# Kernel tuning notes

Measured on AMD Instinct MI355X. Metric: run time of the kernel, lower is better.

The kernel has to match this reference:

```python
import jax, jax.numpy as jnp
import numpy as np
from itertools import permutations

NUM_LAYERS = 3
K = 5  # fixed node degree -> every Hungarian sub-problem is 5x5
# one-hot permutation tensor: P1H[p, r, c] = 1 iff permutation p assigns row r -> col c
PERMS = np.array(list(permutations(range(K))), dtype=np.int32)          # [120, K]
P1H = (PERMS[:, :, None] == np.arange(K)[None, None, :]).astype(np.float32)  # [120, K, K]


def _mlp(x, W1, b1, W2, b2):
    # 2-layer MLP with ReLU (repo's MLP(in, hid, out, 2))
    return jax.nn.relu(x @ W1 + b1) @ W2 + b2


def _sinkhorn(src, itera):
    s = jax.nn.softmax(src, axis=1)  # row-max subtraction is built in
    for i in range(itera):
        s = s / jnp.sum(s, axis=i % 2, keepdims=True)
    return jnp.nan_to_num(s)


def _masked_softmax(src):
    s1 = jnp.nan_to_num(jax.nn.softmax(src, axis=1))
    s2 = jnp.nan_to_num(jax.nn.softmax(src, axis=0))
    return (s1 + s2) * 0.5


def setup_inputs() -> dict:
    key = jax.random.key(0)
    ks = jax.random.split(key, 12)
    n1 = n2 = 1024
    hid = 64
    adj1 = jax.random.randint(ks[0], (n1, K), 0, n1)
    adj2 = jax.random.randint(ks[1], (n2, K), 0, n2)
    # adjacency matrices consistent with the neighbor lists
    G1 = jnp.zeros((n1, n1), jnp.float32).at[jnp.arange(n1)[:, None], adj1].set(1.0)
    G2 = jnp.zeros((n2, n2), jnp.float32).at[jnp.arange(n2)[:, None], adj2].set(1.0)
    s = 0.1
    return {
        'G1': G1, 'G2': G2, 'adj1': adj1, 'adj2': adj2,
        'ro_W1': jax.random.normal(ks[2], (NUM_LAYERS, 1, hid), jnp.float32) * s,
        'ro_b1': jax.random.normal(ks[3], (NUM_LAYERS, hid), jnp.float32) * s,
        'ro_W2': jax.random.normal(ks[4], (NUM_LAYERS, hid, 1), jnp.float32) * s,
        'ro_b2': jax.random.normal(ks[5], (NUM_LAYERS, 1), jnp.float32) * s,
        'fin_W1': jax.random.normal(ks[6], (1, hid), jnp.float32) * s,
        'fin_b1': jax.random.normal(ks[7], (hid,), jnp.float32) * s,
        'fin_W2': jax.random.normal(ks[8], (hid, 1), jnp.float32) * s,
        'fin_b2': jax.random.normal(ks[9], (1,), jnp.float32) * s,
    }


def reference(G1, G2, adj1, adj2, ro_W1, ro_b1, ro_W2, ro_b2, fin_W1, fin_b1, fin_W2, fin_b2):
    n1 = G1.shape[0]
    n2 = G2.shape[0]
    d1 = jnp.sum(G1, axis=1)
    d2 = jnp.sum(G2, axis=1)
    ttheta = jnp.mean(d1)
    # S[i, j, 0] = -|d1[i] - d2[j]|
    S = -jnp.abs(d1[:, None] - d2[None, :])[..., None]  # [n1, n2, 1]
    p1h = jnp.asarray(P1H)
    for li in range(NUM_LAYERS):
        Wn = _sinkhorn(_mlp(S / ttheta, ro_W1[li], ro_b1[li], ro_W2[li], ro_b2[li]).squeeze(-1), 5)
        W = jnp.log(Wn * (n1 * 1.5))
        W = jnp.where(jnp.isneginf(W), jnp.float32(-1e12), W)
        W = jnp.where(jnp.isposinf(W), jnp.float32(1e12), W)
        Wd = jax.lax.stop_gradient(W)  # matches W.detach().numpy()
        # small[a, b, r, c] = Wd[adj1[a, r], adj2[b, c]]  -> [n1, n2, K, K]
        small = jnp.transpose(Wd[adj1][:, :, adj2], (0, 2, 1, 3))
        # exact linear_sum_assignment(-small): maximize sum over the K! permutations
        scores = jnp.einsum('abrc,prc->abp', small, p1h)  # [n1, n2, 120]
        X1 = jnp.max(scores, axis=-1)                      # [n1, n2]
        S = X1[..., None]
    out = _masked_softmax(_mlp(S, fin_W1, fin_b1, fin_W2, fin_b2).squeeze(-1))
    return out
```

## Files before the change

### kernel.cpp

```cpp
#include <hip/hip_runtime.h>
#include <math.h>

#define N 1024
#define NB 256
#define KD 5
#define SL 8
#define NT 126
#define NTP 136
#define MAGIC 0x13572468
#define FSTRIDE 32
#define NGO 32
#define FREGION (NB * FSTRIDE + NGO * FSTRIDE)


__device__ __forceinline__ float load_sc(const float* p){
  return __hip_atomic_load(p, __ATOMIC_RELAXED, __HIP_MEMORY_SCOPE_AGENT);
}
__device__ __forceinline__ void store_sc(float* p, float v){
  __hip_atomic_store(p, v, __ATOMIC_RELAXED, __HIP_MEMORY_SCOPE_AGENT);
}
__device__ __forceinline__ int load_sci(const int* p){
  return __hip_atomic_load(p, __ATOMIC_RELAXED, __HIP_MEMORY_SCOPE_AGENT);
}
__device__ __forceinline__ void store_sci(int* p, int v){
  __hip_atomic_store(p, v, __ATOMIC_RELAXED, __HIP_MEMORY_SCOPE_AGENT);
}

__device__ __forceinline__ void gbar_arrive(int* flg){
  __builtin_amdgcn_s_waitcnt(0);
  __syncthreads();
  if (blockIdx.x != 0 && threadIdx.x == 0)
    store_sci(&flg[blockIdx.x * FSTRIDE], MAGIC);
}
__device__ __forceinline__ void gbar_wait(int* flg){
  const int t = threadIdx.x, B = blockIdx.x;
  int* go = flg + NB * FSTRIDE;
  if (B == 0){
    if (t > 0 && t < NB){
      while (load_sci(&flg[t * FSTRIDE]) != MAGIC) __builtin_amdgcn_s_sleep(1);
    }
    __syncthreads();
    if (t < NGO) store_sci(&go[t * FSTRIDE], MAGIC);
  } else {
    if (t == 0){
      while (load_sci(&go[(B & (NGO - 1)) * FSTRIDE]) != MAGIC) __builtin_amdgcn_s_sleep(1);
    }
    __syncthreads();
  }
}
__device__ __forceinline__ void gbarS(int* flg){ gbar_arrive(flg); gbar_wait(flg); }

__device__ __forceinline__ float wred_sum(float v){
#pragma unroll
  for (int off = 32; off > 0; off >>= 1) v += __shfl_down(v, off);
  return v;
}
__device__ __forceinline__ void bsum4(float v[4], float* s64){
  float w0 = wred_sum(v[0]), w1 = wred_sum(v[1]), w2 = wred_sum(v[2]), w3 = wred_sum(v[3]);
  __syncthreads();
  int wv = threadIdx.x >> 6;
  if ((threadIdx.x & 63) == 0){ s64[wv*4] = w0; s64[wv*4+1] = w1; s64[wv*4+2] = w2; s64[wv*4+3] = w3; }
  __syncthreads();
  float r0 = 0.f, r1 = 0.f, r2 = 0.f, r3 = 0.f;
  const float4* s4 = (const float4*)s64;
#pragma unroll
  for (int i = 0; i < 16; ++i){
    float4 vv = s4[i];
    r0 += vv.x; r1 += vv.y; r2 += vv.z; r3 += vv.w;
  }
  v[0] = r0; v[1] = r1; v[2] = r2; v[3] = r3;
}

__device__ __forceinline__ int distinct5(const int* v){
  int c = 0;
#pragma unroll
  for (int r = 0; r < KD; ++r){
    bool dup = false;
#pragma unroll
    for (int s = 0; s < r; ++s) dup = dup || (v[s] == v[r]);
    c += dup ? 0 : 1;
  }
  return c;
}
__device__ __forceinline__ void sort5(int* s){
#pragma unroll
  for (int i = 0; i < 4; ++i)
#pragma unroll
    for (int j = 0; j < 4 - i; ++j){
      int a = s[j], b = s[j+1];
      s[j] = min(a, b); s[j+1] = max(a, b);
    }
}
__device__ __forceinline__ int msrank(const int* c5){
  const int C_[6][5] = { {0,0,0,0,0},
                         {1,1,1,1,1},
                         {1,2,3,4,5},
                         {1,3,6,10,15},
                         {1,4,10,20,35},
                         {1,5,15,35,70} };
  int rank = 0, prev = 0;
#pragma unroll
  for (int i = 0; i < 5; ++i){
    for (int v = prev; v < c5[i]; ++v) rank += C_[5 - v][4 - i];
    prev = c5[i];
  }
  return rank;
}

#define DP5(ACCESS, OUT) {                                        \
  float f[32]; f[0] = 0.f;                                        \
  _Pragma("unroll")                                               \
  for (int r = 0; r < KD; ++r){                                   \
    float tr[KD];                                                 \
    _Pragma("unroll")                                             \
    for (int c = 0; c < KD; ++c) tr[c] = (ACCESS);                \
    _Pragma("unroll")                                             \
    for (int m = 1; m < 32; ++m){                                 \
      if (__popc(m) == r + 1){                                    \
        float dpb = 0.f; bool dpi = true;                         \
        _Pragma("unroll")                                         \
        for (int c = 0; c < KD; ++c)                              \
          if (m & (1 << c)){                                      \
            float dpv = f[m ^ (1 << c)] + tr[c];                  \
            dpb = dpi ? dpv : fmaxf(dpb, dpv);                    \
            dpi = false;                                          \
          }                                                       \
        f[m] = dpb;                                               \
      }                                                           \
    }                                                             \
  }                                                               \
  OUT = f[31];                                                    \
}

__device__ __forceinline__ void pwl_build(int t,
    const float* __restrict__ w1g, const float* __restrict__ b1g,
    const float* __restrict__ w2g, const float* __restrict__ b2g,
    float* ux, float* udA, float* udB,
    float* xss, float* dAs, float* dBs,
    float* Atb, float* Btb, float* sA0B0)
{
  if (t < 64){
    float w1 = w1g[t], bb = b1g[t], w2v = w2g[t];
    float xk, sdA, sdB, a0t = 0.f, b0t = 0.f;
    if (w1 != 0.f){
      xk = -bb / w1;
      float dA = w1 * w2v, dB = bb * w2v;
      if (w1 > 0.f){ sdA = dA;  sdB = dB; }
      else         { sdA = -dA; sdB = -dB; a0t = dA; b0t = dB; }
    } else {
      xk = 3.0e38f; sdA = 0.f; sdB = 0.f;
      b0t = fmaxf(bb, 0.f) * w2v;
    }
    ux[t] = xk; udA[t] = sdA; udB[t] = sdB;
    float A0 = wred_sum(a0t);
    float B0 = wred_sum(b0t);
    if (t == 0){ sA0B0[0] = A0; sA0B0[1] = B0 + b2g[0]; }
  }
  __syncthreads();
  if (t < 64){
    float xk = ux[t]; int rank = 0;
    for (int j = 0; j < 64; ++j){
      float xj = ux[j];
      rank += (xj < xk || (xj == xk && j < t)) ? 1 : 0;
    }
    xss[rank] = ux[t]; dAs[rank] = udA[t]; dBs[rank] = udB[t];
  }
  __syncthreads();
  if (t < 65){
    float sa = sA0B0[0], sb = sA0B0[1];
    for (int r = 0; r < t; ++r){ sa += dAs[r]; sb += dBs[r]; }
    Atb[t] = sa; Btb[t] = sb;
  }
  __syncthreads();
}

__global__ __launch_bounds__(1024) void
kFused(const int* __restrict__ adj1, const int* __restrict__ adj2,
       const float* __restrict__ roW1, const float* __restrict__ roB1,
       const float* __restrict__ roW2, const float* __restrict__ roB2,
       const float* __restrict__ fW1, const float* __restrict__ fB1,
       const float* __restrict__ fW2, const float* __restrict__ fB2,
       float* __restrict__ tY1g,
       float* __restrict__ C1B, float* __restrict__ C2B, float* __restrict__ C3B,
       float* __restrict__ CFB, float* __restrict__ Rg,
       float* __restrict__ outp,
       int* __restrict__ flg)
{
  __shared__ __align__(16) char uS[20 * N * 4 + N * 4];
  float* tY1 = (float*)uS;
  float (*rows20)[N] = (float (*)[N])uS;
  float* lc = (float*)(uS + 20 * N * 4);
  __shared__ unsigned char t2c[NT][5];
  __shared__ unsigned char sg1[N], sg2[N];
  __shared__ unsigned short st1[N], st2[N];
  __shared__ int h1[8], h2[8];
  __shared__ int cnt1T[NT], cnt2T[NT];
  __shared__ float A1[NT], B1[NT];
  __shared__ float sY0[25], slR0[5], slC0[5], stt2[2];
  __shared__ float slR1[NT], slC1[NT];
  __shared__ float vq[NT], vC[NT], vqi[NT], vCi[NT];
  __shared__ __align__(16) float s64[64];
  __shared__ float sAv[4];
  __shared__ float ux[64], udA[64], udB[64], xss[64], dAs[64], dBs[64];
  __shared__ float Atb[65], Btb[65], sA0B0[2];
  __shared__ float xs3[64], A3t[65], B3t[65];

  const int t = threadIdx.x, B = blockIdx.x;
  const float L1536 = logf(1536.0f);

  if (t < 8){ h1[t] = 0; h2[t] = 0; }
  if (t < NT){ cnt1T[t] = 0; cnt2T[t] = 0; }
#pragma unroll 1
  for (int key = t; key < 3125; key += 1024){
    int d[5]; int k2 = key;
#pragma unroll
    for (int i = 0; i < 5; ++i){ d[i] = k2 % 5; k2 /= 5; }
    if (d[0] <= d[1] && d[1] <= d[2] && d[2] <= d[3] && d[3] <= d[4]){
      int r = msrank(d);
#pragma unroll
      for (int i = 0; i < 5; ++i) t2c[r][i] = (unsigned char)d[i];
    }
  }
  int a2[KD], a1v[KD];
#pragma unroll
  for (int c = 0; c < KD; ++c) a2[c] = adj2[t * KD + c];
#pragma unroll
  for (int r = 0; r < KD; ++r) a1v[r] = adj1[t * KD + r];
  {
    int c2 = distinct5(a2) - 1, c1 = distinct5(a1v) - 1;
    sg2[t] = (unsigned char)c2; sg1[t] = (unsigned char)c1;
#pragma unroll
    for (int k = 0; k < 5; ++k){
      unsigned long long m1 = __ballot(c1 == k);
      unsigned long long m2 = __ballot(c2 == k);
      if ((t & 63) == 0){
        if (m1) atomicAdd(&h1[k], (int)__popcll(m1));
        if (m2) atomicAdd(&h2[k], (int)__popcll(m2));
      }
    }
  }
  __syncthreads();

  {
    int c5[KD];
#pragma unroll
    for (int r = 0; r < KD; ++r) c5[r] = sg1[a1v[r]];
    sort5(c5);
    int ty = msrank(c5);
    st1[t] = (unsigned short)ty; atomicAdd(&cnt1T[ty], 1);
  }
  {
    int c5[KD];
#pragma unroll
    for (int c = 0; c < KD; ++c) c5[c] = sg2[a2[c]];
    sort5(c5);
// ... 79 lines not shown
      stt2[0] = tt;
    }
  } else if (t < 128){
    int l = t - 64;
    const float* w1g = roW1 + 64;
    const float* b1g = roB1 + 64;
    const float* w2g = roW2 + 64;
    const float* b2g = roB2 + 1;
    float w1 = w1g[l], bb = b1g[l], w2v = w2g[l];
    float xk, sdA, sdB, a0t = 0.f, b0t = 0.f;
    if (w1 != 0.f){
      xk = -bb / w1;
      float dA = w1 * w2v, dB = bb * w2v;
      if (w1 > 0.f){ sdA = dA;  sdB = dB; }
      else         { sdA = -dA; sdB = -dB; a0t = dA; b0t = dB; }
    } else {
      xk = 3.0e38f; sdA = 0.f; sdB = 0.f;
      b0t = fmaxf(bb, 0.f) * w2v;
    }
    ux[l] = xk; udA[l] = sdA; udB[l] = sdB;
    float A0 = wred_sum(a0t);
    float B0 = wred_sum(b0t);
    if (l == 0){ sA0B0[0] = A0; sA0B0[1] = B0 + b2g[0]; }
  }
  __syncthreads();

  if (t < 64){
    float xk = ux[t]; int rank = 0;
    for (int j = 0; j < 64; ++j){
      float xj = ux[j];
      rank += (xj < xk || (xj == xk && j < t)) ? 1 : 0;
    }
    xss[rank] = ux[t]; dAs[rank] = udA[t]; dBs[rank] = udB[t];
  } else if (t >= 256 && t < 256 + NT){
    int ty = t - 256;
    float sa = 5.0f * L1536, sb = 0.f;
#pragma unroll
    for (int i = 0; i < KD; ++i){
      int cl = t2c[ty][i];
      sa += slR0[cl];
      sb -= slC0[cl];
    }
    A1[ty] = sa; B1[ty] = sb;
  }
  __syncthreads();
  if (t < 65){
    float sa = sA0B0[0], sb = sA0B0[1];
    for (int r = 0; r < t; ++r){ sa += dAs[r]; sb += dBs[r]; }
    Atb[t] = sa; Btb[t] = sb;
  }
  __syncthreads();

  const float tt = stt2[0];
  if (t < 63){
    int e = B + 256 * t;
    if (e < NT * NT){
      int tau = e / NT, ups = e - tau * NT;
      const unsigned char* G = t2c[tau];
      const unsigned char* H = t2c[ups];
      float D;
      DP5(sY0[(int)G[r] * 5 + (int)H[c]], D);
      float x = (A1[tau] + B1[ups] + D) / tt;
      int seg = 0;
#pragma unroll
      for (int s = 64; s; s >>= 1)
        if (seg + s <= 64 && xss[seg + s - 1] <= x) seg += s;
      store_sc(&tY1g[e], fmaf(Atb[seg], x, Btb[seg]));
    }
  }

  gbar_arrive(flg + 0 * FREGION);
  pwl_build(t, fW1, fB1, fW2, fB2,
            ux, udA, udB, xs3, dAs, dBs, A3t, B3t, sA0B0);
  pwl_build(t, roW1 + 128, roB1 + 128, roW2 + 128, roB2 + 2,
            ux, udA, udB, xss, dAs, dBs, Atb, Btb, sA0B0);
  gbar_wait(flg + 0 * FREGION);

  float rv[16];
  int lidx[16];
#pragma unroll
  for (int i = 0; i < 16; ++i){
    int e = t + 1024 * i;
    if (e < NT * NT){
      rv[i] = load_sc(&tY1g[e]);
      lidx[i] = e + (NTP - NT) * (e / NT);
    }
  }
#pragma unroll
  for (int i = 0; i < 16; ++i){
    int e = t + 1024 * i;
    if (e < NT * NT) tY1[lidx[i]] = rv[i];
  }
  __syncthreads();

  int stc[KD];
#pragma unroll
  for (int c = 0; c < KD; ++c) stc[c] = st2[a2[c]];
  float D2[4];
#pragma unroll 1
  for (int rr = 0; rr < 4; ++rr){
    int str_[KD];
#pragma unroll
    for (int r = 0; r < KD; ++r) str_[r] = st1[adj1[(4 * B + rr) * KD + r]];
    float D;
    DP5(tY1[str_[r] * NTP + stc[c]], D);
    D2[rr] = D;
  }
  __syncthreads();
#pragma unroll
  for (int i = 0; i < 16; ++i){
    int e = t + 1024 * i;
    if (e < NT * NT) tY1[lidx[i]] = expf(rv[i]);
  }
  __syncthreads();

  {
    int g = t >> 3, j = t & 7;
    float Er[16], Ec[16];
    if (g < NT){
#pragma unroll
      for (int i = 0; i < 16; ++i){
        int u = j + 8 * i;
        if (u < NT){
          Er[i] = (float)cnt2T[u] * tY1[g * NTP + u];
          Ec[i] = (float)cnt1T[u] * tY1[u * NTP + g];
        } else { Er[i] = 0.f; Ec[i] = 0.f; }
      }
    }
    if (g < NT){
      float acc = 0.f;
#pragma unroll
      for (int i = 0; i < 16; ++i){ int u = j + 8 * i; if (u < NT) acc += Er[i]; }
      acc += __shfl_down(acc, 4, 8); acc += __shfl_down(acc, 2, 8); acc += __shfl_down(acc, 1, 8);
      if (j == 0){ vq[g] = acc; vqi[g] = 1.0f / acc; }
    }
    __syncthreads();
    if (g < NT){
      float acc = 0.f;
#pragma unroll
      for (int i = 0; i < 16; ++i){ int u = j + 8 * i; if (u < NT) acc += Ec[i] * vqi[u]; }
      acc += __shfl_down(acc, 4, 8); acc += __shfl_down(acc, 2, 8); acc += __shfl_down(acc, 1, 8);
      if (j == 0){ vC[g] = acc; vCi[g] = 1.0f / acc; }
    }
    __syncthreads();
    if (g < NT){
      float acc = 0.f;
#pragma unroll
      for (int i = 0; i < 16; ++i){ int u = j + 8 * i; if (u < NT) acc += Er[i] * vCi[u]; }
      acc += __shfl_down(acc, 4, 8); acc += __shfl_down(acc, 2, 8); acc += __shfl_down(acc, 1, 8);
      if (j == 0){ vq[g] = acc; vqi[g] = 1.0f / acc; }
    }
    __syncthreads();
    if (g < NT){
      float acc = 0.f;
#pragma unroll
      for (int i = 0; i < 16; ++i){ int u = j + 8 * i; if (u < NT) acc += Ec[i] * vqi[u]; }
      acc += __shfl_down(acc, 4, 8); acc += __shfl_down(acc, 2, 8); acc += __shfl_down(acc, 1, 8);
      if (j == 0){ vC[g] = acc; vCi[g] = 1.0f / acc; }
    }
    __syncthreads();
    if (g < NT){
      float acc = 0.f;
#pragma unroll
      for (int i = 0; i < 16; ++i){ int u = j + 8 * i; if (u < NT) acc += Er[i] * vCi[u]; }
      acc += __shfl_down(acc, 4, 8); acc += __shfl_down(acc, 2, 8); acc += __shfl_down(acc, 1, 8);
      if (j == 0){ vq[g] = acc; vqi[g] = 1.0f / acc; }
    }
    __syncthreads();
    if (g < NT){
      float acc = 0.f;
#pragma unroll
      for (int i = 0; i < 16; ++i){ int u = j + 8 * i; if (u < NT) acc += Ec[i] * vqi[u]; }
      acc += __shfl_down(acc, 4, 8); acc += __shfl_down(acc, 2, 8); acc += __shfl_down(acc, 1, 8);
      if (j == 0) vC[g] = acc;
    }
    __syncthreads();
  }
  if (t < NT){ slR1[t] = -logf(vq[t]); slC1[t] = logf(vC[t]); }
  __syncthreads();

  if (t < 4){
    int a = 4 * B + t;
    float s = 5.0f * L1536;
#pragma unroll
    for (int r = 0; r < KD; ++r) s += slR1[st1[adj1[a * KD + r]]];
    sAv[t] = s;
  }
  float Bv2 = 0.f;
#pragma unroll
  for (int c = 0; c < KD; ++c) Bv2 -= slC1[stc[c]];
  __syncthreads();

  float y2[4];
#pragma unroll
  for (int rr = 0; rr < 4; ++rr){
    float x = (sAv[rr] + Bv2 + D2[rr]) / tt;
    int seg = 0;
#pragma unroll
    for (int s = 64; s; s >>= 1)
      if (seg + s <= 64 && xss[seg + s - 1] <= x) seg += s;
    y2[rr] = fmaf(Atb[seg], x, Btb[seg]);
  }
  float E[4], q4[4];
#pragma unroll
  for (int r = 0; r < 4; ++r){ E[r] = expf(y2[r]); q4[r] = E[r]; }
  bsum4(q4, s64);
  {
    float cp = 0.f;
#pragma unroll
    for (int r = 0; r < 4; ++r){
      store_sc(&outp[(size_t)(4 * B + r) * N + t], y2[r]);
      cp += E[r] / q4[r];
    }
    atomicAdd(&C1B[(size_t)(B & (SL - 1)) * N + t], cp);
  }

  gbarS(flg + 1 * FREGION);

  float rv20[20];
#pragma unroll
  for (int k = 0; k < 20; ++k){
    int src = adj1[(4 * B + (k / 5)) * KD + (k % 5)];
    rv20[k] = load_sc(&outp[(size_t)src * N + t]);
  }

  {
    float C = 0.f;
#pragma unroll
    for (int k = 0; k < SL; ++k) C += load_sc(&C1B[(size_t)k * N + t]);
    float iC = 1.0f / C;
#pragma unroll
    for (int r = 0; r < 4; ++r) q4[r] = E[r] * iC;
    bsum4(q4, s64);
    float cp = 0.f;
#pragma unroll
    for (int r = 0; r < 4; ++r) cp += E[r] / q4[r];
    atomicAdd(&C2B[(size_t)(B & (SL - 1)) * N + t], cp);
  }

  gbar_arrive(flg + 2 * FREGION);
#pragma unroll
  for (int k = 0; k < 20; ++k) rows20[k][t] = rv20[k];
  __syncthreads();
  float D3[4];
#pragma unroll 1
  for (int rr = 0; rr < 4; ++rr){
    float D;
    DP5(rows20[rr * 5 + r][a2[c]], D);
    D3[rr] = D;
  }
  gbar_wait(flg + 2 * FREGION);

  {
    float C = 0.f;
#pragma unroll
    for (int k = 0; k < SL; ++k) C += load_sc(&C2B[(size_t)k * N + t]);
    float iC = 1.0f / C;
#pragma unroll
    for (int r = 0; r < 4; ++r) q4[r] = E[r] * iC;
    bsum4(q4, s64);
    float cp = 0.f;
#pragma unroll
    for (int r = 0; r < 4; ++r) cp += E[r] / q4[r];
    if (t < 4) store_sc(&Rg[4 * B + t], 1.0f / q4[t]);
    atomicAdd(&C3B[(size_t)(B & (SL - 1)) * N + t], cp);
  }

  gbarS(flg + 3 * FREGION);
  {
    float C = 0.f;
#pragma unroll
    for (int k = 0; k < SL; ++k) C += load_sc(&C3B[(size_t)k * N + t]);
    lc[t] = logf(C);
  }
  if (t >= 64 && t < 68){
    int a = 4 * B + (t - 64);
    float s = 5.0f * logf(1536.0f);
#pragma unroll
    for (int r = 0; r < KD; ++r) s += logf(load_sc(&Rg[adj1[a * KD + r]]));
    sAv[t - 64] = s;
  }
  __syncthreads();

  float Bvl = 0.f;
#pragma unroll
  for (int c = 0; c < KD; ++c) Bvl -= lc[a2[c]];

  float y[4];
#pragma unroll
  for (int rr = 0; rr < 4; ++rr){
    float x = sAv[rr] + Bvl + D3[rr];
    int seg = 0;
#pragma unroll
    for (int s = 64; s; s >>= 1)
      if (seg + s <= 64 && xs3[seg + s - 1] <= x) seg += s;
    y[rr] = fmaf(A3t[seg], x, B3t[seg]);
  }

  float e4[4];
#pragma unroll
  for (int r = 0; r < 4; ++r){ e4[r] = expf(y[r]); q4[r] = e4[r]; }
  bsum4(q4, s64);

  {
    float cp = 0.f;
#pragma unroll
    for (int r = 0; r < 4; ++r) cp += e4[r];
    atomicAdd(&CFB[(size_t)(B & (SL - 1)) * N + t], cp);
  }

  gbar_arrive(flg + 4 * FREGION);
  float iq[4];
#pragma unroll
  for (int r = 0; r < 4; ++r) iq[r] = 1.0f / q4[r];
  gbar_wait(flg + 4 * FREGION);

  float CF = 0.f;
#pragma unroll
  for (int k = 0; k < SL; ++k) CF += load_sc(&CFB[(size_t)k * N + t]);
  float iCF = 1.0f / CF;
#pragma unroll
  for (int r = 0; r < 4; ++r){
    float v = 0.5f * e4[r] * (iq[r] + iCF);
    outp[(size_t)(4 * B + r) * N + t] = v;
  }
}

extern "C" void kernel_launch(void* const* d_in, const int* in_sizes, int n_in,
                              void* d_out, int out_size, void* d_ws, size_t ws_size,
                              hipStream_t stream){
  (void)in_sizes; (void)n_in; (void)out_size; (void)ws_size;
  const int*   adj1 = (const int*)d_in[2];
  const int*   adj2 = (const int*)d_in[3];
  const float* roW1 = (const float*)d_in[4];
  const float* roB1 = (const float*)d_in[5];
  const float* roW2 = (const float*)d_in[6];
  const float* roB2 = (const float*)d_in[7];
  const float* fW1  = (const float*)d_in[8];
  const float* fB1  = (const float*)d_in[9];
  const float* fW2  = (const float*)d_in[10];
  const float* fB2  = (const float*)d_in[11];
  float* out = (float*)d_out;

  float* Pp   = (float*)d_ws;
  float* Rg   = Pp + (size_t)4 * SL * N;
  float* tY1g = Rg + N;
  int*   flg  = (int*)(tY1g + NT * NT);

  kFused<<<NB, 1024, 0, stream>>>(adj1, adj2, roW1, roB1, roW2, roB2,
                                  fW1, fB1, fW2, fB2,
                                  tY1g,
                                  Pp + (size_t)0 * SL * N, Pp + (size_t)1 * SL * N,
                                  Pp + (size_t)2 * SL * N, Pp + (size_t)3 * SL * N,
                                  Rg, out, flg);
}
```

Before: 146.9 us.

## Double grid to 512 blocks with two rows each and shrink shared memory

Raises the persistent grid from 256 to 512 blocks, so each block now handles two output rows instead of four. Shared memory is cut by dropping the padded tY1 layout, shrinking the row buffer and aliasing several small arrays, so two 1024-thread blocks can fit per CU. The intent is more parallelism and less serial per-block work on a 256-CU GPU. In exchange, the global barriers must wait on twice as many blocks, there are more atomic adds, and removing the padding may bring back LDS bank conflicts.

```diff
diff --git a/kernel.cpp b/kernel.cpp
--- a/kernel.cpp
+++ b/kernel.cpp
@@ -2,11 +2,10 @@
 #include <math.h>
 
 #define N 1024
-#define NB 256
+#define NB 512
 #define KD 5
 #define SL 8
 #define NT 126
-#define NTP 136
 #define MAGIC 0x13572468
 #define FSTRIDE 32
 #define NGO 32
@@ -55,20 +54,17 @@
   for (int off = 32; off > 0; off >>= 1) v += __shfl_down(v, off);
   return v;
 }
-__device__ __forceinline__ void bsum4(float v[4], float* s64){
-  float w0 = wred_sum(v[0]), w1 = wred_sum(v[1]), w2 = wred_sum(v[2]), w3 = wred_sum(v[3]);
+__device__ __forceinline__ void bsum2(float v[2], float* s64){
+  float w0 = wred_sum(v[0]), w1 = wred_sum(v[1]);
   __syncthreads();
   int wv = threadIdx.x >> 6;
-  if ((threadIdx.x & 63) == 0){ s64[wv*4] = w0; s64[wv*4+1] = w1; s64[wv*4+2] = w2; s64[wv*4+3] = w3; }
-  __syncthreads();
-  float r0 = 0.f, r1 = 0.f, r2 = 0.f, r3 = 0.f;
-  const float4* s4 = (const float4*)s64;
-#pragma unroll
-  for (int i = 0; i < 16; ++i){
-    float4 vv = s4[i];
-    r0 += vv.x; r1 += vv.y; r2 += vv.z; r3 += vv.w;
-  }
-  v[0] = r0; v[1] = r1; v[2] = r2; v[3] = r3;
+  if ((threadIdx.x & 63) == 0){ s64[wv*2] = w0; s64[wv*2+1] = w1; }
+  __syncthreads();
+  float r0 = 0.f, r1 = 0.f;
+  const float2* s2 = (const float2*)s64;
+#pragma unroll
+  for (int i = 0; i < 16; ++i){ float2 vv = s2[i]; r0 += vv.x; r1 += vv.y; }
+  v[0] = r0; v[1] = r1;
 }
 
 __device__ __forceinline__ int distinct5(const int* v){
@@ -174,7 +170,7 @@
   __syncthreads();
 }
 
-__global__ __launch_bounds__(1024) void
+__global__ __launch_bounds__(1024, 8) void
 kFused(const int* __restrict__ adj1, const int* __restrict__ adj2,
        const float* __restrict__ roW1, const float* __restrict__ roB1,
        const float* __restrict__ roW2, const float* __restrict__ roB2,
@@ -186,21 +182,27 @@
        float* __restrict__ outp,
        int* __restrict__ flg)
 {
-  __shared__ __align__(16) char uS[20 * N * 4 + N * 4];
+  __shared__ __align__(16) char uS[NT * NT * 4];
   float* tY1 = (float*)uS;
-  float (*rows20)[N] = (float (*)[N])uS;
-  float* lc = (float*)(uS + 20 * N * 4);
+  float (*rows10)[N] = (float (*)[N])uS;
+  float* lc = (float*)(uS + 10 * N * 4);
+  __shared__ __align__(16) unsigned char sgU[2048];
+  unsigned char* sg1 = sgU;
+  unsigned char* sg2 = sgU + 1024;
+  float* vq  = (float*)sgU;
+  float* vC  = vq + NT;
+  float* vqi = vC + NT;
+  float* vCi = vqi + NT;
+  __shared__ float AB1U[2 * NT];
+  float* A1 = AB1U;         float* B1 = AB1U + NT;
+  float* slR1 = AB1U;       float* slC1 = AB1U + NT;
   __shared__ unsigned char t2c[NT][5];
-  __shared__ unsigned char sg1[N], sg2[N];
   __shared__ unsigned short st1[N], st2[N];
   __shared__ int h1[8], h2[8];
   __shared__ int cnt1T[NT], cnt2T[NT];
-  __shared__ float A1[NT], B1[NT];
   __shared__ float sY0[25], slR0[5], slC0[5], stt2[2];
-  __shared__ float slR1[NT], slC1[NT];
-  __shared__ float vq[NT], vC[NT], vqi[NT], vCi[NT];
   __shared__ __align__(16) float s64[64];
-  __shared__ float sAv[4];
+  __shared__ float sAv[2];
   __shared__ float ux[64], udA[64], udB[64], xss[64], dAs[64], dBs[64];
   __shared__ float Atb[65], Btb[65], sA0B0[2];
   __shared__ float xs3[64], A3t[65], B3t[65];
@@ -386,8 +388,8 @@
   __syncthreads();
 
   const float tt = stt2[0];
-  if (t < 63){
-    int e = B + 256 * t;
+  if (t < 32){
+    int e = B + 512 * t;
     if (e < NT * NT){
       int tau = e / NT, ups = e - tau * NT;
       const unsigned char* G = t2c[tau];
@@ -411,40 +413,36 @@
   gbar_wait(flg + 0 * FREGION);
 
   float rv[16];
-  int lidx[16];
 #pragma unroll
   for (int i = 0; i < 16; ++i){
     int e = t + 1024 * i;
-    if (e < NT * NT){
-      rv[i] = load_sc(&tY1g[e]);
-      lidx[i] = e + (NTP - NT) * (e / NT);
-    }
+    if (e < NT * NT) rv[i] = load_sc(&tY1g[e]);
   }
 #pragma unroll
   for (int i = 0; i < 16; ++i){
     int e = t + 1024 * i;
-    if (e < NT * NT) tY1[lidx[i]] = rv[i];
+    if (e < NT * NT) tY1[e] = rv[i];
   }
   __syncthreads();
 
   int stc[KD];
 #pragma unroll
   for (int c = 0; c < KD; ++c) stc[c] = st2[a2[c]];
-  float D2[4];
+  float D2[2];
 #pragma unroll 1
-  for (int rr = 0; rr < 4; ++rr){
+  for (int rr = 0; rr < 2; ++rr){
     int str_[KD];
 #pragma unroll
-    for (int r = 0; r < KD; ++r) str_[r] = st1[adj1[(4 * B + rr) * KD + r]];
+    for (int r = 0; r < KD; ++r) str_[r] = st1[adj1[(2 * B + rr) * KD + r]];
     float D;
-    DP5(tY1[str_[r] * NTP + stc[c]], D);
+    DP5(tY1[str_[r] * NT + stc[c]], D);
     D2[rr] = D;
   }
   __syncthreads();
 #pragma unroll
   for (int i = 0; i < 16; ++i){
     int e = t + 1024 * i;
-    if (e < NT * NT) tY1[lidx[i]] = expf(rv[i]);
+    if (e < NT * NT) tY1[e] = expf(rv[i]);
   }
   __syncthreads();
 
@@ -456,8 +454,8 @@
       for (int i = 0; i < 16; ++i){
         int u = j + 8 * i;
         if (u < NT){
-          Er[i] = (float)cnt2T[u] * tY1[g * NTP + u];
-          Ec[i] = (float)cnt1T[u] * tY1[u * NTP + g];
+          Er[i] = (float)cnt2T[u] * tY1[g * NT + u];
+          Ec[i] = (float)cnt1T[u] * tY1[u * NT + g];
         } else { Er[i] = 0.f; Ec[i] = 0.f; }
       }
     }
@@ -513,8 +511,8 @@
   if (t < NT){ slR1[t] = -logf(vq[t]); slC1[t] = logf(vC[t]); }
   __syncthreads();
 
-  if (t < 4){
-    int a = 4 * B + t;
+  if (t < 2){
+    int a = 2 * B + t;
     float s = 5.0f * L1536;
 #pragma unroll
     for (int r = 0; r < KD; ++r) s += slR1[st1[adj1[a * KD + r]]];
@@ -525,9 +523,9 @@
   for (int c = 0; c < KD; ++c) Bv2 -= slC1[stc[c]];
   __syncthreads();
 
-  float y2[4];
-#pragma unroll
-  for (int rr = 0; rr < 4; ++rr){
+  float y2[2];
+#pragma unroll
+  for (int rr = 0; rr < 2; ++rr){
     float x = (sAv[rr] + Bv2 + D2[rr]) / tt;
     int seg = 0;
 #pragma unroll
@@ -535,15 +533,15 @@
       if (seg + s <= 64 && xss[seg + s - 1] <= x) seg += s;
     y2[rr] = fmaf(Atb[seg], x, Btb[seg]);
   }
-  float E[4], q4[4];
-#pragma unroll
-  for (int r = 0; r < 4; ++r){ E[r] = expf(y2[r]); q4[r] = E[r]; }
-  bsum4(q4, s64);
+  float E[2], q4[2];
+#pragma unroll
+  for (int r = 0; r < 2; ++r){ E[r] = expf(y2[r]); q4[r] = E[r]; }
+  bsum2(q4, s64);
   {
     float cp = 0.f;
 #pragma unroll
-    for (int r = 0; r < 4; ++r){
-      store_sc(&outp[(size_t)(4 * B + r) * N + t], y2[r]);
+    for (int r = 0; r < 2; ++r){
+      store_sc(&outp[(size_t)(2 * B + r) * N + t], y2[r]);
       cp += E[r] / q4[r];
     }
     atomicAdd(&C1B[(size_t)(B & (SL - 1)) * N + t], cp);
@@ -551,11 +549,11 @@
 
   gbarS(flg + 1 * FREGION);
 
-  float rv20[20];
-#pragma unroll
-  for (int k = 0; k < 20; ++k){
-    int src = adj1[(4 * B + (k / 5)) * KD + (k % 5)];
-    rv20[k] = load_sc(&outp[(size_t)src * N + t]);
+  float rv10[10];
+#pragma unroll
+  for (int k = 0; k < 10; ++k){
+    int src = adj1[(2 * B + (k / 5)) * KD + (k % 5)];
+    rv10[k] = load_sc(&outp[(size_t)src * N + t]);
   }
 
   {
@@ -564,23 +562,23 @@
     for (int k = 0; k < SL; ++k) C += load_sc(&C1B[(size_t)k * N + t]);
     float iC = 1.0f / C;
 #pragma unroll
-    for (int r = 0; r < 4; ++r) q4[r] = E[r] * iC;
-    bsum4(q4, s64);
+    for (int r = 0; r < 2; ++r) q4[r] = E[r] * iC;
+    bsum2(q4, s64);
     float cp = 0.f;
 #pragma unroll
-    for (int r = 0; r < 4; ++r) cp += E[r] / q4[r];
+    for (int r = 0; r < 2; ++r) cp += E[r] / q4[r];
     atomicAdd(&C2B[(size_t)(B & (SL - 1)) * N + t], cp);
   }
 
   gbar_arrive(flg + 2 * FREGION);
 #pragma unroll
-  for (int k = 0; k < 20; ++k) rows20[k][t] = rv20[k];
-  __syncthreads();
-  float D3[4];
+  for (int k = 0; k < 10; ++k) rows10[k][t] = rv10[k];
+  __syncthreads();
+  float D3[2];
 #pragma unroll 1
-  for (int rr = 0; rr < 4; ++rr){
+  for (int rr = 0; rr < 2; ++rr){
     float D;
-    DP5(rows20[rr * 5 + r][a2[c]], D);
+    DP5(rows10[rr * 5 + r][a2[c]], D);
     D3[rr] = D;
   }
   gbar_wait(flg + 2 * FREGION);
@@ -591,12 +589,12 @@
     for (int k = 0; k < SL; ++k) C += load_sc(&C2B[(size_t)k * N + t]);
     float iC = 1.0f / C;
 #pragma unroll
-    for (int r = 0; r < 4; ++r) q4[r] = E[r] * iC;
-    bsum4(q4, s64);
+    for (int r = 0; r < 2; ++r) q4[r] = E[r] * iC;
+    bsum2(q4, s64);
     float cp = 0.f;
 #pragma unroll
-    for (int r = 0; r < 4; ++r) cp += E[r] / q4[r];
-    if (t < 4) store_sc(&Rg[4 * B + t], 1.0f / q4[t]);
+    for (int r = 0; r < 2; ++r) cp += E[r] / q4[r];
+    if (t < 2) store_sc(&Rg[2 * B + t], 1.0f / q4[t]);
     atomicAdd(&C3B[(size_t)(B & (SL - 1)) * N + t], cp);
   }
 
@@ -607,8 +605,8 @@
     for (int k = 0; k < SL; ++k) C += load_sc(&C3B[(size_t)k * N + t]);
     lc[t] = logf(C);
   }
-  if (t >= 64 && t < 68){
-    int a = 4 * B + (t - 64);
+  if (t >= 64 && t < 66){
+    int a = 2 * B + (t - 64);
     float s = 5.0f * logf(1536.0f);
 #pragma unroll
     for (int r = 0; r < KD; ++r) s += logf(load_sc(&Rg[adj1[a * KD + r]]));
@@ -620,9 +618,9 @@
 #pragma unroll
   for (int c = 0; c < KD; ++c) Bvl -= lc[a2[c]];
 
-  float y[4];
-#pragma unroll
-  for (int rr = 0; rr < 4; ++rr){
+  float y[2];
+#pragma unroll
+  for (int rr = 0; rr < 2; ++rr){
     float x = sAv[rr] + Bvl + D3[rr];
     int seg = 0;
 #pragma unroll
@@ -631,22 +629,22 @@
     y[rr] = fmaf(A3t[seg], x, B3t[seg]);
   }
 
-  float e4[4];
-#pragma unroll
-  for (int r = 0; r < 4; ++r){ e4[r] = expf(y[r]); q4[r] = e4[r]; }
-  bsum4(q4, s64);
+  float e4[2];
+#pragma unroll
+  for (int r = 0; r < 2; ++r){ e4[r] = expf(y[r]); q4[r] = e4[r]; }
+  bsum2(q4, s64);
 
   {
     float cp = 0.f;
 #pragma unroll
-    for (int r = 0; r < 4; ++r) cp += e4[r];
+    for (int r = 0; r < 2; ++r) cp += e4[r];
     atomicAdd(&CFB[(size_t)(B & (SL - 1)) * N + t], cp);
   }
 
   gbar_arrive(flg + 4 * FREGION);
-  float iq[4];
-#pragma unroll
-  for (int r = 0; r < 4; ++r) iq[r] = 1.0f / q4[r];
+  float iq[2];
+#pragma unroll
+  for (int r = 0; r < 2; ++r) iq[r] = 1.0f / q4[r];
   gbar_wait(flg + 4 * FREGION);
 
   float CF = 0.f;
@@ -654,9 +652,9 @@
   for (int k = 0; k < SL; ++k) CF += load_sc(&CFB[(size_t)k * N + t]);
   float iCF = 1.0f / CF;
 #pragma unroll
-  for (int r = 0; r < 4; ++r){
+  for (int r = 0; r < 2; ++r){
     float v = 0.5f * e4[r] * (iq[r] + iCF);
-    outp[(size_t)(4 * B + r) * N + t] = v;
+    outp[(size_t)(2 * B + r) * N + t] = v;
   }
 }
 
```

After: 169.6 us. 1.15x slower.

## Add 512-block persistent kernel variant with two rows per block

Applied to the files above, without the earlier changes.

Adds a second fused kernel that launches 512 blocks of 1024 threads. Each block handles two rows instead of four, register use is capped at 64 VGPRs, and shared memory is cut so two blocks can fit per CU. The host queries occupancy and picks this variant when two blocks can be resident, otherwise it falls back to the original 256-block kernel. The aim is to double resident waves and halve per-block serial work. The cost is a larger grid barrier (512 flags polled by block 0), plus risk of register spills or a deadlock if the occupancy query overstates residency.

```diff
diff --git a/kernel.cpp b/kernel.cpp
--- a/kernel.cpp
+++ b/kernel.cpp
@@ -2,7 +2,6 @@
 #include <math.h>
 
 #define N 1024
-#define NB 256
 #define KD 5
 #define SL 8
 #define NT 126
@@ -10,7 +9,8 @@
 #define MAGIC 0x13572468
 #define FSTRIDE 32
 #define NGO 32
-#define FREGION (NB * FSTRIDE + NGO * FSTRIDE)
+#define FREG512 (512 * FSTRIDE + NGO * FSTRIDE)
+#define FREG256 (256 * FSTRIDE + NGO * FSTRIDE)
 
 
 __device__ __forceinline__ float load_sc(const float* p){
@@ -32,11 +32,11 @@
   if (blockIdx.x != 0 && threadIdx.x == 0)
     store_sci(&flg[blockIdx.x * FSTRIDE], MAGIC);
 }
-__device__ __forceinline__ void gbar_wait(int* flg){
+__device__ __forceinline__ void gbar_wait(int* flg, int nb){
   const int t = threadIdx.x, B = blockIdx.x;
-  int* go = flg + NB * FSTRIDE;
+  int* go = flg + nb * FSTRIDE;
   if (B == 0){
-    if (t > 0 && t < NB){
+    if (t > 0 && t < nb){
       while (load_sci(&flg[t * FSTRIDE]) != MAGIC) __builtin_amdgcn_s_sleep(1);
     }
     __syncthreads();
@@ -48,12 +48,23 @@
     __syncthreads();
   }
 }
-__device__ __forceinline__ void gbarS(int* flg){ gbar_arrive(flg); gbar_wait(flg); }
 
 __device__ __forceinline__ float wred_sum(float v){
 #pragma unroll
   for (int off = 32; off > 0; off >>= 1) v += __shfl_down(v, off);
   return v;
+}
+__device__ __forceinline__ void bsum2(float v[2], float* s64){
+  float w0 = wred_sum(v[0]), w1 = wred_sum(v[1]);
+  __syncthreads();
+  int wv = threadIdx.x >> 6;
+  if ((threadIdx.x & 63) == 0){ s64[wv*2] = w0; s64[wv*2+1] = w1; }
+  __syncthreads();
+  float r0 = 0.f, r1 = 0.f;
+  const float2* s2 = (const float2*)s64;
+#pragma unroll
+  for (int i = 0; i < 16; ++i){ float2 vv = s2[i]; r0 += vv.x; r1 += vv.y; }
+  v[0] = r0; v[1] = r1;
 }
 __device__ __forceinline__ void bsum4(float v[4], float* s64){
   float w0 = wred_sum(v[0]), w1 = wred_sum(v[1]), w2 = wred_sum(v[2]), w3 = wred_sum(v[3]);
@@ -174,17 +185,510 @@
   __syncthreads();
 }
 
+
+__global__ __launch_bounds__(1024) __attribute__((amdgpu_num_vgpr(64))) void
+kF512(const int* __restrict__ adj1, const int* __restrict__ adj2,
+      const float* __restrict__ roW1, const float* __restrict__ roB1,
+      const float* __restrict__ roW2, const float* __restrict__ roB2,
+      const float* __restrict__ fW1, const float* __restrict__ fB1,
+      const float* __restrict__ fW2, const float* __restrict__ fB2,
+      float* __restrict__ tY1g,
+      float* __restrict__ C1B, float* __restrict__ C2B, float* __restrict__ C3B,
+      float* __restrict__ CFB, float* __restrict__ Rg,
+      float* __restrict__ outp,
+      int* __restrict__ flg)
+{
+  __shared__ __align__(16) char uS[NT * NT * 4];
+  float* tY1 = (float*)uS;
+  float (*rows10)[N] = (float (*)[N])uS;
+  float* lc = (float*)(uS + 10 * N * 4);
+  __shared__ __align__(16) unsigned char sgU[2048];
+  unsigned char* sg1 = sgU;
+  unsigned char* sg2 = sgU + 1024;
+  float* vq  = (float*)sgU;
+  float* vC  = vq + NT;
+  float* vqi = vC + NT;
+  float* vCi = vqi + NT;
+  __shared__ float AB1U[2 * NT];
+  float* A1 = AB1U;         float* B1 = AB1U + NT;
+  float* slR1 = AB1U;       float* slC1 = AB1U + NT;
+  __shared__ unsigned char t2c[NT][5];
+  __shared__ unsigned short st1[N], st2[N];
+  __shared__ int h1[8], h2[8];
+  __shared__ int cnt1T[NT], cnt2T[NT];
+  __shared__ float sY0[25], slR0[5], slC0[5], stt2[2];
+  __shared__ __align__(16) float s64[64];
+  __shared__ float sAv[2];
+  __shared__ float ux[64], udA[64], udB[64], xss[64], dAs[64], dBs[64];
+  __shared__ float Atb[65], Btb[65], sA0B0[2];
+  __shared__ float xs3[64], A3t[65], B3t[65];
+
+  const int t = threadIdx.x, B = blockIdx.x;
+  const float L1536 = logf(1536.0f);
+
+  if (t < 8){ h1[t] = 0; h2[t] = 0; }
+  if (t < NT){ cnt1T[t] = 0; cnt2T[t] = 0; }
+#pragma unroll 1
+  for (int key = t; key < 3125; key += 1024){
+    int d[5]; int k2 = key;
+#pragma unroll
+    for (int i = 0; i < 5; ++i){ d[i] = k2 % 5; k2 /= 5; }
+    if (d[0] <= d[1] && d[1] <= d[2] && d[2] <= d[3] && d[3] <= d[4]){
+      int r = msrank(d);
+#pragma unroll
+      for (int i = 0; i < 5; ++i) t2c[r][i] = (unsigned char)d[i];
+    }
+  }
+  int a2[KD], a1v[KD];
+#pragma unroll
+  for (int c = 0; c < KD; ++c) a2[c] = adj2[t * KD + c];
+#pragma unroll
+  for (int r = 0; r < KD; ++r) a1v[r] = adj1[t * KD + r];
+  {
+    int c2 = distinct5(a2) - 1, c1 = distinct5(a1v) - 1;
+    sg2[t] = (unsigned char)c2; sg1[t] = (unsigned char)c1;
+#pragma unroll
+    for (int k = 0; k < 5; ++k){
+      unsigned long long m1 = __ballot(c1 == k);
+      unsigned long long m2 = __ballot(c2 == k);
+      if ((t & 63) == 0){
+        if (m1) atomicAdd(&h1[k], (int)__popcll(m1));
+        if (m2) atomicAdd(&h2[k], (int)__popcll(m2));
+      }
+    }
+  }
+  __syncthreads();
+
+  {
+    int c5[KD];
+#pragma unroll
+    for (int r = 0; r < KD; ++r) c5[r] = sg1[a1v[r]];
+    sort5(c5);
+    int ty = msrank(c5);
+    st1[t] = (unsigned short)ty; atomicAdd(&cnt1T[ty], 1);
+  }
+  {
+    int c5[KD];
+#pragma unroll
+    for (int c = 0; c < KD; ++c) c5[c] = sg2[a2[c]];
+    sort5(c5);
+    int ty = msrank(c5);
+    st2[t] = (unsigned short)ty; atomicAdd(&cnt2T[ty], 1);
+  }
+
+  if (t < 64){
+    float cnt1[5], cnt2[5];
+#pragma unroll
+    for (int g = 0; g < 5; ++g){ cnt1[g] = (float)h1[g]; cnt2[g] = (float)h2[g]; }
+    float tt = 0.f;
+#pragma unroll
+    for (int g = 0; g < 5; ++g) tt += (float)(g + 1) * cnt1[g];
+    tt *= (1.0f / 1024.0f);
+    float tab[5];
+#pragma unroll 1
+    for (int i = 0; i < 5; ++i){
+      float x = -(float)i / tt;
+      float acc = roB2[0];
+      for (int k = 0; k < 64; ++k){
+        float hh = fmaxf(fmaf(x, roW1[k], roB1[k]), 0.f);
+        acc = fmaf(hh, roW2[k], acc);
+      }
+      tab[i] = acc;
+    }
+    float Ee[5][5];
+#pragma unroll
+    for (int g = 0; g < 5; ++g)
+#pragma unroll
+      for (int h = 0; h < 5; ++h) Ee[g][h] = expf(tab[abs(g - h)]);
+    float q0[5], C1c[5], q1[5], C2c[5], q2[5], C3c[5];
+#pragma unroll
+    for (int g = 0; g < 5; ++g){
+      float s = 0.f;
+#pragma unroll
+      for (int h = 0; h < 5; ++h) s += cnt2[h] * Ee[g][h];
+      q0[g] = s;
+    }
+#pragma unroll
+    for (int h = 0; h < 5; ++h){
+      float s = 0.f;
+#pragma unroll
+      for (int g = 0; g < 5; ++g) s += cnt1[g] * Ee[g][h] / q0[g];
+      C1c[h] = s;
+    }
+#pragma unroll
+    for (int g = 0; g < 5; ++g){
+      float s = 0.f;
+#pragma unroll
+      for (int h = 0; h < 5; ++h) s += cnt2[h] * Ee[g][h] / C1c[h];
+      q1[g] = s;
+    }
+#pragma unroll
+    for (int h = 0; h < 5; ++h){
+      float s = 0.f;
+#pragma unroll
+      for (int g = 0; g < 5; ++g) s += cnt1[g] * Ee[g][h] / q1[g];
+      C2c[h] = s;
+    }
+#pragma unroll
+    for (int g = 0; g < 5; ++g){
+      float s = 0.f;
+#pragma unroll
+      for (int h = 0; h < 5; ++h) s += cnt2[h] * Ee[g][h] / C2c[h];
+      q2[g] = s;
+    }
+#pragma unroll
+    for (int h = 0; h < 5; ++h){
+      float s = 0.f;
+#pragma unroll
+      for (int g = 0; g < 5; ++g) s += cnt1[g] * Ee[g][h] / q2[g];
+      C3c[h] = s;
+    }
+    if (t == 0){
+#pragma unroll
+      for (int g = 0; g < 5; ++g){
+#pragma unroll
+        for (int h = 0; h < 5; ++h) sY0[g * 5 + h] = tab[abs(g - h)];
+        slR0[g] = -logf(q2[g]);
+        slC0[g] = logf(C3c[g]);
+      }
+      stt2[0] = tt;
+    }
+  } else if (t < 128){
+    int l = t - 64;
+    const float* w1g = roW1 + 64;
+    const float* b1g = roB1 + 64;
+    const float* w2g = roW2 + 64;
+    const float* b2g = roB2 + 1;
+    float w1 = w1g[l], bb = b1g[l], w2v = w2g[l];
+    float xk, sdA, sdB, a0t = 0.f, b0t = 0.f;
+    if (w1 != 0.f){
+      xk = -bb / w1;
+      float dA = w1 * w2v, dB = bb * w2v;
+      if (w1 > 0.f){ sdA = dA;  sdB = dB; }
+      else         { sdA = -dA; sdB = -dB; a0t = dA; b0t = dB; }
+    } else {
+      xk = 3.0e38f; sdA = 0.f; sdB = 0.f;
+      b0t = fmaxf(bb, 0.f) * w2v;
+    }
+    ux[l] = xk; udA[l] = sdA; udB[l] = sdB;
+    float A0 = wred_sum(a0t);
+    float B0 = wred_sum(b0t);
+    if (l == 0){ sA0B0[0] = A0; sA0B0[1] = B0 + b2g[0]; }
+  }
+  __syncthreads();
+
+  if (t < 64){
+    float xk = ux[t]; int rank = 0;
+    for (int j = 0; j < 64; ++j){
+      float xj = ux[j];
+      rank += (xj < xk || (xj == xk && j < t)) ? 1 : 0;
+    }
+    xss[rank] = ux[t]; dAs[rank] = udA[t]; dBs[rank] = udB[t];
+  } else if (t >= 256 && t < 256 + NT){
+    int ty = t - 256;
+    float sa = 5.0f * L1536, sb = 0.f;
+#pragma unroll
+    for (int i = 0; i < KD; ++i){
+      int cl = t2c[ty][i];
+      sa += slR0[cl];
+      sb -= slC0[cl];
+    }
+    A1[ty] = sa; B1[ty] = sb;
+  }
+  __syncthreads();
+  if (t < 65){
+    float sa = sA0B0[0], sb = sA0B0[1];
+    for (int r = 0; r < t; ++r){ sa += dAs[r]; sb += dBs[r]; }
+    Atb[t] = sa; Btb[t] = sb;
+  }
+  __syncthreads();
+
+  const float tt = stt2[0];
+  if (t < 32){
+    int e = B + 512 * t;
+    if (e < NT * NT){
+      int tau = e / NT, ups = e - tau * NT;
+      const unsigned char* G = t2c[tau];
+      const unsigned char* H = t2c[ups];
+      float D;
+      DP5(sY0[(int)G[r] * 5 + (int)H[c]], D);
+      float x = (A1[tau] + B1[ups] + D) / tt;
+      int seg = 0;
+#pragma unroll
+      for (int s = 64; s; s >>= 1)
+        if (seg + s <= 64 && xss[seg + s - 1] <= x) seg += s;
+      store_sc(&tY1g[e], fmaf(Atb[seg], x, Btb[seg]));
+    }
+  }
+
+  gbar_arrive(flg + 0 * FREG512);
+  pwl_build(t, fW1, fB1, fW2, fB2,
+            ux, udA, udB, xs3, dAs, dBs, A3t, B3t, sA0B0);
+  pwl_build(t, roW1 + 128, roB1 + 128, roW2 + 128, roB2 + 2,
+            ux, udA, udB, xss, dAs, dBs, Atb, Btb, sA0B0);
+  gbar_wait(flg + 0 * FREG512, 512);
+
+  {
+    float rv[16];
+#pragma unroll
+    for (int i = 0; i < 16; ++i){
+      int e = t + 1024 * i;
+      if (e < NT * NT) rv[i] = load_sc(&tY1g[e]);
+    }
+#pragma unroll
+    for (int i = 0; i < 16; ++i){
+      int e = t + 1024 * i;
+      if (e < NT * NT) tY1[e] = rv[i];
+    }
+  }
+  __syncthreads();
+
+  int stc[KD];
+#pragma unroll
+  for (int c = 0; c < KD; ++c) stc[c] = st2[a2[c]];
+  float D2[2];
+#pragma unroll 1
+  for (int rr = 0; rr < 2; ++rr){
+    int str_[KD];
+#pragma unroll
+    for (int r = 0; r < KD; ++r) str_[r] = st1[adj1[(2 * B + rr) * KD + r]];
+    float D;
+    DP5(tY1[str_[r] * NT + stc[c]], D);
+    D2[rr] = D;
+  }
+  __syncthreads();
+#pragma unroll
+  for (int i = 0; i < 16; ++i){
+    int e = t + 1024 * i;
+    if (e < NT * NT){ float lv = tY1[e]; tY1[e] = expf(lv); }
+  }
+  __syncthreads();
+
+  {
+    int g = t >> 3, j = t & 7;
+    float Er[16], Ec[16];
+    if (g < NT){
+#pragma unroll
+      for (int i = 0; i < 16; ++i){
+        int u = j + 8 * i;
+        if (u < NT){
+          Er[i] = (float)cnt2T[u] * tY1[g * NT + u];
+          Ec[i] = (float)cnt1T[u] * tY1[u * NT + g];
+        } else { Er[i] = 0.f; Ec[i] = 0.f; }
+      }
+    }
+    if (g < NT){
+      float acc = 0.f;
+#pragma unroll
+      for (int i = 0; i < 16; ++i){ int u = j + 8 * i; if (u < NT) acc += Er[i]; }
+      acc += __shfl_down(acc, 4, 8); acc += __shfl_down(acc, 2, 8); acc += __shfl_down(acc, 1, 8);
+      if (j == 0){ vq[g] = acc; vqi[g] = 1.0f / acc; }
+    }
+    __syncthreads();
+    if (g < NT){
+      float acc = 0.f;
+#pragma unroll
+      for (int i = 0; i < 16; ++i){ int u = j + 8 * i; if (u < NT) acc += Ec[i] * vqi[u]; }
+      acc += __shfl_down(acc, 4, 8); acc += __shfl_down(acc, 2, 8); acc += __shfl_down(acc, 1, 8);
+      if (j == 0){ vC[g] = acc; vCi[g] = 1.0f / acc; }
+    }
+    __syncthreads();
+    if (g < NT){
+      float acc = 0.f;
+#pragma unroll
+      for (int i = 0; i < 16; ++i){ int u = j + 8 * i; if (u < NT) acc += Er[i] * vCi[u]; }
+      acc += __shfl_down(acc, 4, 8); acc += __shfl_down(acc, 2, 8); acc += __shfl_down(acc, 1, 8);
+      if (j == 0){ vq[g] = acc; vqi[g] = 1.0f / acc; }
+    }
+    __syncthreads();
+    if (g < NT){
+      float acc = 0.f;
+#pragma unroll
+      for (int i = 0; i < 16; ++i){ int u = j + 8 * i; if (u < NT) acc += Ec[i] * vqi[u]; }
+      acc += __shfl_down(acc, 4, 8); acc += __shfl_down(acc, 2, 8); acc += __shfl_down(acc, 1, 8);
+      if (j == 0){ vC[g] = acc; vCi[g] = 1.0f / acc; }
+    }
+    __syncthreads();
+    if (g < NT){
+      float acc = 0.f;
+#pragma unroll
+      for (int i = 0; i < 16; ++i){ int u = j + 8 * i; if (u < NT) acc += Er[i] * vCi[u]; }
+      acc += __shfl_down(acc, 4, 8); acc += __shfl_down(acc, 2, 8); acc += __shfl_down(acc, 1, 8);
+      if (j == 0){ vq[g] = acc; vqi[g] = 1.0f / acc; }
+    }
+    __syncthreads();
+    if (g < NT){
+      float acc = 0.f;
+#pragma unroll
+      for (int i = 0; i < 16; ++i){ int u = j + 8 * i; if (u < NT) acc += Ec[i] * vqi[u]; }
+      acc += __shfl_down(acc, 4, 8); acc += __shfl_down(acc, 2, 8); acc += __shfl_down(acc, 1, 8);
+      if (j == 0) vC[g] = acc;
+    }
+    __syncthreads();
+  }
+  if (t < NT){ slR1[t] = -logf(vq[t]); slC1[t] = logf(vC[t]); }
+  __syncthreads();
+
+  if (t < 2){
+    int a = 2 * B + t;
+    float s = 5.0f * L1536;
+#pragma unroll
+    for (int r = 0; r < KD; ++r) s += slR1[st1[adj1[a * KD + r]]];
+    sAv[t] = s;
+  }
+  float Bv2 = 0.f;
+#pragma unroll
+  for (int c = 0; c < KD; ++c) Bv2 -= slC1[stc[c]];
+  __syncthreads();
+
+  float y2[2];
+#pragma unroll
+  for (int rr = 0; rr < 2; ++rr){
+    float x = (sAv[rr] + Bv2 + D2[rr]) / tt;
+    int seg = 0;
+#pragma unroll
+    for (int s = 64; s; s >>= 1)
+      if (seg + s <= 64 && xss[seg + s - 1] <= x) seg += s;
+    y2[rr] = fmaf(Atb[seg], x, Btb[seg]);
+  }
+  float E[2], q4[2];
+#pragma unroll
+  for (int r = 0; r < 2; ++r){ E[r] = expf(y2[r]); q4[r] = E[r]; }
+  bsum2(q4, s64);
+  {
+    float cp = 0.f;
+#pragma unroll
+    for (int r = 0; r < 2; ++r){
+      store_sc(&outp[(size_t)(2 * B + r) * N + t], y2[r]);
+      cp += E[r] / q4[r];
+    }
+    atomicAdd(&C1B[(size_t)(B & (SL - 1)) * N + t], cp);
+  }
+
+  gbar_arrive(flg + 1 * FREG512);
+  gbar_wait(flg + 1 * FREG512, 512);
+
+  float rv10[10];
+#pragma unroll
+  for (int k = 0; k < 10; ++k){
+    int src = adj1[(2 * B + (k / 5)) * KD + (k % 5)];
+    rv10[k] = load_sc(&outp[(size_t)src * N + t]);
+  }
+
+  {
+    float C = 0.f;
+#pragma unroll
+    for (int k = 0; k < SL; ++k) C += load_sc(&C1B[(size_t)k * N + t]);
+    float iC = 1.0f / C;
+#pragma unroll
+    for (int r = 0; r < 2; ++r) q4[r] = E[r] * iC;
+    bsum2(q4, s64);
+    float cp = 0.f;
+#pragma unroll
+    for (int r = 0; r < 2; ++r) cp += E[r] / q4[r];
+    atomicAdd(&C2B[(size_t)(B & (SL - 1)) * N + t], cp);
+  }
+
+  gbar_arrive(flg + 2 * FREG512);
+#pragma unroll
+  for (int k = 0; k < 10; ++k) rows10[k][t] = rv10[k];
+  __syncthreads();
+  float D3[2];
+#pragma unroll 1
+  for (int rr = 0; rr < 2; ++rr){
+    float D;
+    DP5(rows10[rr * 5 + r][a2[c]], D);
+    D3[rr] = D;
+  }
+  gbar_wait(flg + 2 * FREG512, 512);
+
+  {
+    float C = 0.f;
+#pragma unroll
+    for (int k = 0; k < SL; ++k) C += load_sc(&C2B[(size_t)k * N + t]);
+    float iC = 1.0f / C;
+#pragma unroll
+    for (int r = 0; r < 2; ++r) q4[r] = E[r] * iC;
+    bsum2(q4, s64);
+    float cp = 0.f;
+#pragma unroll
+    for (int r = 0; r < 2; ++r) cp += E[r] / q4[r];
+    if (t < 2) store_sc(&Rg[2 * B + t], 1.0f / q4[t]);
+    atomicAdd(&C3B[(size_t)(B & (SL - 1)) * N + t], cp);
+  }
+
+  gbar_arrive(flg + 3 * FREG512);
+  gbar_wait(flg + 3 * FREG512, 512);
+  {
+    float C = 0.f;
+#pragma unroll
+    for (int k = 0; k < SL; ++k) C += load_sc(&C3B[(size_t)k * N + t]);
+    lc[t] = logf(C);
+  }
+  if (t >= 64 && t < 66){
+    int a = 2 * B + (t - 64);
+    float s = 5.0f * logf(1536.0f);
+#pragma unroll
+    for (int r = 0; r < KD; ++r) s += logf(load_sc(&Rg[adj1[a * KD + r]]));
+    sAv[t - 64] = s;
+  }
+  __syncthreads();
+
+  float Bvl = 0.f;
+#pragma unroll
+  for (int c = 0; c < KD; ++c) Bvl -= lc[a2[c]];
+
+  float y[2];
+#pragma unroll
+  for (int rr = 0; rr < 2; ++rr){
+    float x = sAv[rr] + Bvl + D3[rr];
+    int seg = 0;
+#pragma unroll
+    for (int s = 64; s; s >>= 1)
+      if (seg + s <= 64 && xs3[seg + s - 1] <= x) seg += s;
+    y[rr] = fmaf(A3t[seg], x, B3t[seg]);
+  }
+
+  float e4[2];
+#pragma unroll
+  for (int r = 0; r < 2; ++r){ e4[r] = expf(y[r]); q4[r] = e4[r]; }
+  bsum2(q4, s64);
+
+  {
+    float cp = 0.f;
+#pragma unroll
+    for (int r = 0; r < 2; ++r) cp += e4[r];
+    atomicAdd(&CFB[(size_t)(B & (SL - 1)) * N + t], cp);
+  }
+
+  gbar_arrive(flg + 4 * FREG512);
+  float iq[2];
+#pragma unroll
+  for (int r = 0; r < 2; ++r) iq[r] = 1.0f / q4[r];
+  gbar_wait(flg + 4 * FREG512, 512);
+
+  float CF = 0.f;
+#pragma unroll
+  for (int k = 0; k < SL; ++k) CF += load_sc(&CFB[(size_t)k * N + t]);
+  float iCF = 1.0f / CF;
+#pragma unroll
+  for (int r = 0; r < 2; ++r){
+    float v = 0.5f * e4[r] * (iq[r] + iCF);
+    outp[(size_t)(2 * B + r) * N + t] = v;
+  }
+}
+
 __global__ __launch_bounds__(1024) void
-kFused(const int* __restrict__ adj1, const int* __restrict__ adj2,
-       const float* __restrict__ roW1, const float* __restrict__ roB1,
-       const float* __restrict__ roW2, const float* __restrict__ roB2,
-       const float* __restrict__ fW1, const float* __restrict__ fB1,
-       const float* __restrict__ fW2, const float* __restrict__ fB2,
-       float* __restrict__ tY1g,
-       float* __restrict__ C1B, float* __restrict__ C2B, float* __restrict__ C3B,
-       float* __restrict__ CFB, float* __restrict__ Rg,
-       float* __restrict__ outp,
-       int* __restrict__ flg)
+kF256(const int* __restrict__ adj1, const int* __restrict__ adj2,
+      const float* __restrict__ roW1, const float* __restrict__ roB1,
+      const float* __restrict__ roW2, const float* __restrict__ roB2,
+      const float* __restrict__ fW1, const float* __restrict__ fB1,
+      const float* __restrict__ fW2, const float* __restrict__ fB2,
+      float* __restrict__ tY1g,
+      float* __restrict__ C1B, float* __restrict__ C2B, float* __restrict__ C3B,
+      float* __restrict__ CFB, float* __restrict__ Rg,
+      float* __restrict__ outp,
+      int* __restrict__ flg)
 {
   __shared__ __align__(16) char uS[20 * N * 4 + N * 4];
   float* tY1 = (float*)uS;
@@ -403,12 +907,12 @@
     }
   }
 
-  gbar_arrive(flg + 0 * FREGION);
+  gbar_arrive(flg + 0 * FREG256);
   pwl_build(t, fW1, fB1, fW2, fB2,
             ux, udA, udB, xs3, dAs, dBs, A3t, B3t, sA0B0);
   pwl_build(t, roW1 + 128, roB1 + 128, roW2 + 128, roB2 + 2,
             ux, udA, udB, xss, dAs, dBs, Atb, Btb, sA0B0);
-  gbar_wait(flg + 0 * FREGION);
+  gbar_wait(flg + 0 * FREG256, 256);
 
   float rv[16];
   int lidx[16];
@@ -549,7 +1053,8 @@
     atomicAdd(&C1B[(size_t)(B & (SL - 1)) * N + t], cp);
   }
 
-  gbarS(flg + 1 * FREGION);
+  gbar_arrive(flg + 1 * FREG256);
+  gbar_wait(flg + 1 * FREG256, 256);
 
   float rv20[20];
 #pragma unroll
@@ -572,7 +1077,7 @@
     atomicAdd(&C2B[(size_t)(B & (SL - 1)) * N + t], cp);
   }
 
-  gbar_arrive(flg + 2 * FREGION);
+  gbar_arrive(flg + 2 * FREG256);
 #pragma unroll
   for (int k = 0; k < 20; ++k) rows20[k][t] = rv20[k];
   __syncthreads();
@@ -583,7 +1088,7 @@
     DP5(rows20[rr * 5 + r][a2[c]], D);
     D3[rr] = D;
   }
-  gbar_wait(flg + 2 * FREGION);
+  gbar_wait(flg + 2 * FREG256, 256);
 
   {
     float C = 0.f;
@@ -600,7 +1105,8 @@
     atomicAdd(&C3B[(size_t)(B & (SL - 1)) * N + t], cp);
   }
 
-  gbarS(flg + 3 * FREGION);
+  gbar_arrive(flg + 3 * FREG256);
+  gbar_wait(flg + 3 * FREG256, 256);
   {
     float C = 0.f;
 #pragma unroll
@@ -643,11 +1149,11 @@
     atomicAdd(&CFB[(size_t)(B & (SL - 1)) * N + t], cp);
   }
 
-  gbar_arrive(flg + 4 * FREGION);
+  gbar_arrive(flg + 4 * FREG256);
   float iq[4];
 #pragma unroll
   for (int r = 0; r < 4; ++r) iq[r] = 1.0f / q4[r];
-  gbar_wait(flg + 4 * FREGION);
+  gbar_wait(flg + 4 * FREG256, 256);
 
   float CF = 0.f;
 #pragma unroll
@@ -681,10 +1187,20 @@
   float* tY1g = Rg + N;
   int*   flg  = (int*)(tY1g + NT * NT);
 
-  kFused<<<NB, 1024, 0, stream>>>(adj1, adj2, roW1, roB1, roW2, roB2,
-                                  fW1, fB1, fW2, fB2,
-                                  tY1g,
-                                  Pp + (size_t)0 * SL * N, Pp + (size_t)1 * SL * N,
-                                  Pp + (size_t)2 * SL * N, Pp + (size_t)3 * SL * N,
-                                  Rg, out, flg);
-}
+  int nb2 = 0;
+  hipError_t e = hipOccupancyMaxActiveBlocksPerMultiprocessor(
+      &nb2, reinterpret_cast<const void*>(&kF512), 1024, 0);
+  if (e == hipSuccess && nb2 >= 2){
+    kF512<<<512, 1024, 0, stream>>>(adj1, adj2, roW1, roB1, roW2, roB2,
+                                    fW1, fB1, fW2, fB2, tY1g,
+                                    Pp + (size_t)0 * SL * N, Pp + (size_t)1 * SL * N,
+                                    Pp + (size_t)2 * SL * N, Pp + (size_t)3 * SL * N,
+                                    Rg, out, flg);
+  } else {
+    kF256<<<256, 1024, 0, stream>>>(adj1, adj2, roW1, roB1, roW2, roB2,
+                                    fW1, fB1, fW2, fB2, tY1g,
+                                    Pp + (size_t)0 * SL * N, Pp + (size_t)1 * SL * N,
+                                    Pp + (size_t)2 * SL * N, Pp + (size_t)3 * SL * N,
+                                    Rg, out, flg);
+  }
+}
```

Measured after the change: 147.7 us. About the same (+0.5%).
